# Kernel optimization log

Hardware: AMD Instinct MI355X
Metric: run time of the kernel (lower is better)

The kernel has to match this reference:

```python
import jax, jax.numpy as jnp
import numpy as np

B = 128          # graphs
N = 512          # nodes per graph
NT = B * N       # total nodes = 65536
E = NT * 16      # total edges = 1048576
IN = 64
H = 128
OUT = 2
L = 4            # num_layers
RATIO = 0.8


def setup_inputs() -> dict:
    key = jax.random.key(0)
    ks = jax.random.split(key, 20)

    def w(k, shape, fan_in):
        return jax.random.normal(k, shape, jnp.float32) / np.sqrt(fan_in)

    x = jax.random.normal(ks[0], (NT, IN), jnp.float32)
    edge_index = jax.random.randint(ks[1], (2, E), 0, NT, dtype=jnp.int32)
    batch = (jnp.arange(NT) // N).astype(jnp.int32)  # equal-size graphs

    return {
        "x": x,
        "edge_index": edge_index,
        "batch": batch,
        # conv1: GraphConv(IN, H, aggr='mean') -> lin_rel (w/ bias) + lin_root (no bias)
        "W1_rel": w(ks[2], (IN, H), IN),
        "W1_root": w(ks[3], (IN, H), IN),
        "b1": jnp.zeros((H,), jnp.float32),
        # convs[0..2]: GraphConv(H, H, aggr='mean'), stacked
        "Wc_rel": w(ks[4], (L - 1, H, H), H),
        "Wc_root": w(ks[5], (L - 1, H, H), H),
        "bc": jnp.zeros((L - 1, H), jnp.float32),
        # SAGPooling score GNN: GraphConv(H, 1) with default aggr='add'
        "pw_rel": w(ks[6], (H,), H),
        "pw_root": w(ks[7], (H,), H),
        "pb": jnp.zeros((1,), jnp.float32),
        # MLP head
        "lin1_W": w(ks[8], (L * H, H), L * H),
        "lin1_b": jnp.zeros((H,), jnp.float32),
        "lin2_W": w(ks[9], (H, OUT), H),
        "lin2_b": jnp.zeros((OUT,), jnp.float32),
    }


def _graph_conv_mean(x, src, dst, emask, W_rel, W_root, b, n):
    # PyG GraphConv: lin_rel(mean_{j->i} x_j) + lin_root(x_i); masked edges excluded.
    msg = x[src] * emask[:, None]                                  # [E, D] gather
    s = jax.ops.segment_sum(msg, dst, num_segments=n)              # [n, D] scatter-add
    cnt = jax.ops.segment_sum(emask, dst, num_segments=n)          # [n]
    agg = s / jnp.maximum(cnt, 1.0)[:, None]                       # zero for isolated nodes
    return agg @ W_rel + x @ W_root + b


def reference(x, edge_index, batch, W1_rel, W1_root, b1, Wc_rel, Wc_root, bc,
              pw_rel, pw_root, pb, lin1_W, lin1_b, lin2_W, lin2_b):
    src = edge_index[0]
    dst = edge_index[1]
    emask = jnp.ones((E,), jnp.float32)
    n = NT
    npg = N  # nodes per graph (all graphs equal size)

    h = jax.nn.relu(_graph_conv_mean(x, src, dst, emask, W1_rel, W1_root, b1, n))
    xs = [h.reshape(B, npg, H).mean(axis=1)]  # global_mean_pool

    for i in range(L - 1):
        h = jax.nn.relu(_graph_conv_mean(h, src, dst, emask, Wc_rel[i], Wc_root[i], bc[i], n))
        xs.append(h.reshape(B, npg, H).mean(axis=1))
        if i % 2 == 0 and i < L - 2:
            # ---- SAGPooling: score via GraphConv(H,1) with add aggregation ----
            smsg = jax.ops.segment_sum(h[src] * emask[:, None], dst, num_segments=n)
            score = smsg @ pw_rel + h @ pw_root + pb[0]            # [n]
            k = int(np.ceil(RATIO * npg))
            topv, topi = jax.lax.top_k(score.reshape(B, npg), k)   # per-graph top-k
            perm = (jnp.arange(B)[:, None] * npg + topi).reshape(-1)  # global kept ids
            h = h[perm] * jnp.tanh(topv.reshape(-1))[:, None]
            # remap edges; edges touching dropped nodes get masked out
            node_map = jnp.full((n,), -1, jnp.int32).at[perm].set(
                jnp.arange(B * k, dtype=jnp.int32))
            ns, nd = node_map[src], node_map[dst]
            keep = ((ns >= 0) & (nd >= 0)).astype(jnp.float32)
            emask = emask * keep
            src = jnp.where(ns >= 0, ns, 0)
            dst = jnp.where(nd >= 0, nd, 0)
            n = B * k
            npg = k

    xcat = jnp.concatenate(xs, axis=-1)                            # JumpingKnowledge 'cat'
    out = jax.nn.relu(xcat @ lin1_W + lin1_b)
    # dropout is identity in eval mode
    out = out @ lin2_W + lin2_b
    return jax.nn.log_softmax(out, axis=-1)
```

## Files before the change

kernel.cpp:

```cpp
#include <hip/hip_runtime.h>
#include <math.h>

#define NT 65536
#define EE 1048576
#define NB 128
#define KK 410
#define HH 128

typedef short bf16x8 __attribute__((ext_vector_type(8)));
typedef float f32x4 __attribute__((ext_vector_type(4)));

__device__ unsigned short g_xb[(size_t)NT * 64];
__device__ unsigned short g_hb1[(size_t)NT * HH];
__device__ unsigned short g_hb2[(size_t)NT * HH];
__device__ unsigned short g_aggb[(size_t)NT * HH];
__device__ unsigned short g_hpb[(size_t)NT * HH];
__device__ unsigned short g_aggb64[(size_t)NT * 64];
__device__ unsigned short g_wt1[128 * 128];
__device__ unsigned short g_wtc[3 * 128 * 256];
__device__ unsigned short g_csr1u[EE];
__device__ unsigned short g_keptu[NT];
__device__ unsigned int g_ebuck[EE];
__device__ int g_bcnt[128];
__device__ int g_bbase[129];
__device__ int g_bcur[128];
__device__ float g_trel[NT];
__device__ float g_troot[NT];
__device__ float g_score[NT];
__device__ float g_kinv[NT];
__device__ float g_xc4[4 * NB * 4 * 128];
__device__ int g_rows1[NT + 1];

__device__ __forceinline__ unsigned short* ubuf(int id) {
    switch (id) {
        case 0: return g_xb;
        case 1: return g_hb1;
        case 2: return g_hb2;
        case 3: return g_aggb;
        case 4: return g_hpb;
        case 5: return g_aggb64;
        case 6: return g_wt1;
        case 7: return g_wtc;
    }
    return g_xb;
}

__device__ __forceinline__ float b2f(unsigned short u) {
    union { unsigned int i; float f; } v;
    v.i = ((unsigned int)u) << 16;
    return v.f;
}
__device__ __forceinline__ unsigned short f2b(float f) {
    unsigned int x = __float_as_uint(f);
    unsigned int r = x + 0x7fffu + ((x >> 16) & 1u);
    return (unsigned short)(r >> 16);
}

__global__ void k_prep(const float* __restrict__ x,
                       const float* __restrict__ W1r, const float* __restrict__ W1o,
                       const float* __restrict__ Wcr, const float* __restrict__ Wco) {
    int tid = blockIdx.x * 256 + threadIdx.x;
    if (tid < 1048576) {
        float4 v = *(const float4*)&x[(size_t)tid * 4];
        unsigned int lo = (unsigned int)f2b(v.x) | ((unsigned int)f2b(v.y) << 16);
        unsigned int hi = (unsigned int)f2b(v.z) | ((unsigned int)f2b(v.w) << 16);
        *(uint2*)&g_xb[(size_t)tid * 4] = make_uint2(lo, hi);
    } else if (tid < 1048576 + 16384) {
        int r = tid - 1048576;
        int k = r & 127, n = r >> 7;
        float v = (k < 64) ? W1r[k * 128 + n] : W1o[(k - 64) * 128 + n];
        g_wt1[n * 128 + k] = f2b(v);
    } else if (tid < 1048576 + 16384 + 98304) {
        int r = tid - (1048576 + 16384);
        int l = r >> 15;
        int k = r & 255, n = (r >> 8) & 127;
        float v = (k < 128) ? Wcr[l * 16384 + k * 128 + n]
                            : Wco[l * 16384 + (k - 128) * 128 + n];
        g_wtc[l * 32768 + n * 256 + k] = f2b(v);
    } else if (tid < 1048576 + 16384 + 98304 + 128) {
        g_bcnt[tid - (1048576 + 16384 + 98304)] = 0;
    }
}

__global__ __launch_bounds__(256) void k_bhist(const int* __restrict__ dst) {
    __shared__ int h[128];
    if (threadIdx.x < 128) h[threadIdx.x] = 0;
    __syncthreads();
    int e0 = (blockIdx.x * 256 + threadIdx.x) * 4;
    int4 d = *(const int4*)&dst[e0];
    atomicAdd(&h[d.x >> 9], 1);
    atomicAdd(&h[d.y >> 9], 1);
    atomicAdd(&h[d.z >> 9], 1);
    atomicAdd(&h[d.w >> 9], 1);
    __syncthreads();
    if (threadIdx.x < 128 && h[threadIdx.x]) atomicAdd(&g_bcnt[threadIdx.x], h[threadIdx.x]);
}

__global__ __launch_bounds__(128) void k_bscan() {
    __shared__ int s[128];
    int t = threadIdx.x;
    int v = g_bcnt[t];
    s[t] = v;
    __syncthreads();
    for (int off = 1; off < 128; off <<= 1) {
        int u = (t >= off) ? s[t - off] : 0;
        __syncthreads();
        s[t] += u;
        __syncthreads();
    }
    g_bbase[t] = s[t] - v;
    g_bcur[t] = s[t] - v;
    if (t == 127) g_bbase[128] = s[127];
}

__global__ __launch_bounds__(256) void k_bscatter(const int* __restrict__ src,
                                                  const int* __restrict__ dst) {
    __shared__ int h[128];
    __shared__ int base[128];
    if (threadIdx.x < 128) h[threadIdx.x] = 0;
    __syncthreads();
    int e0 = (blockIdx.x * 256 + threadIdx.x) * 4;
    int4 s = *(const int4*)&src[e0];
    int4 d = *(const int4*)&dst[e0];
    int b0 = d.x >> 9, b1 = d.y >> 9, b2 = d.z >> 9, b3 = d.w >> 9;
    atomicAdd(&h[b0], 1);
    atomicAdd(&h[b1], 1);
    atomicAdd(&h[b2], 1);
    atomicAdd(&h[b3], 1);
    __syncthreads();
    if (threadIdx.x < 128) {
        int c = h[threadIdx.x];
        base[threadIdx.x] = c ? atomicAdd(&g_bcur[threadIdx.x], c) : 0;
        h[threadIdx.x] = 0;
    }
    __syncthreads();
    int r0 = atomicAdd(&h[b0], 1);
    g_ebuck[base[b0] + r0] = ((unsigned int)(d.x & 511) << 16) | (unsigned int)s.x;
    int r1 = atomicAdd(&h[b1], 1);
    g_ebuck[base[b1] + r1] = ((unsigned int)(d.y & 511) << 16) | (unsigned int)s.y;
    int r2 = atomicAdd(&h[b2], 1);
    g_ebuck[base[b2] + r2] = ((unsigned int)(d.z & 511) << 16) | (unsigned int)s.z;
    int r3 = atomicAdd(&h[b3], 1);
    g_ebuck[base[b3] + r3] = ((unsigned int)(d.w & 511) << 16) | (unsigned int)s.w;
}

__global__ __launch_bounds__(512) void k_bcsr() {
    __shared__ int hist[512];
    __shared__ int offs[512];
    __shared__ int cur[512];
    int g = blockIdx.x, t = threadIdx.x;
    hist[t] = 0;
    cur[t] = 0;
    __syncthreads();
    int b0 = g_bbase[g], b1 = g_bbase[g + 1];
    for (int e = b0 + t; e < b1; e += 512) {
        unsigned int p = g_ebuck[e];
        atomicAdd(&hist[p >> 16], 1);
    }
    __syncthreads();
    int v = hist[t];
    offs[t] = v;
    __syncthreads();
    for (int off = 1; off < 512; off <<= 1) {
        int u = (t >= off) ? offs[t - off] : 0;
        __syncthreads();
        offs[t] += u;
        __syncthreads();
    }
    int excl = offs[t] - v;
    g_rows1[g * 512 + t] = b0 + excl;
    if (t == 511) g_rows1[g * 512 + 512] = b0 + excl + v;
    __syncthreads();
    offs[t] = excl;
    __syncthreads();
    for (int e = b0 + t; e < b1; e += 512) {
        unsigned int p = g_ebuck[e];
        int dl = p >> 16;
        int r = atomicAdd(&cur[dl], 1);
        g_csr1u[b0 + offs[dl] + r] = (unsigned short)(p & 0xFFFFu);
    }
}

template <int D, int KC>
__global__ __launch_bounds__(256) void k_agg(int hId, int outId) {
    const unsigned short* h = ubuf(hId);
    unsigned short* out = ubuf(outId);
    const int TPN = D / 8;
    const int npb = 256 / TPN;
    int local = threadIdx.x / TPN;
    int t = threadIdx.x % TPN;
    int node = blockIdx.x * npb + local;
    int r0 = g_rows1[node], r1 = g_rows1[node + 1];
    float kinv_pre = (KC == 2) ? g_kinv[node] : 0.f;
    float acc[8];
#pragma unroll
    for (int i = 0; i < 8; i++) acc[i] = 0.f;
    int kc = 0;
    const unsigned short* ht = h + t * 8;
#define ACCV(v)                                                  \
    acc[0] += b2f((unsigned short)(v.x & 0xffff));               \
    acc[1] += b2f((unsigned short)(v.x >> 16));                  \
    acc[2] += b2f((unsigned short)(v.y & 0xffff));               \
    acc[3] += b2f((unsigned short)(v.y >> 16));                  \
    acc[4] += b2f((unsigned short)(v.z & 0xffff));               \
    acc[5] += b2f((unsigned short)(v.z >> 16));                  \
    acc[6] += b2f((unsigned short)(v.w & 0xffff));               \
    acc[7] += b2f((unsigned short)(v.w >> 16));
    int e = r0;
    for (; e + 8 <= r1; e += 8) {
        int i0 = g_csr1u[e], i1 = g_csr1u[e + 1], i2 = g_csr1u[e + 2], i3 = g_csr1u[e + 3];
        int i4 = g_csr1u[e + 4], i5 = g_csr1u[e + 5], i6 = g_csr1u[e + 6], i7 = g_csr1u[e + 7];
        uint4 v0 = *(const uint4*)&ht[(size_t)i0 * D];
        uint4 v1 = *(const uint4*)&ht[(size_t)i1 * D];
        uint4 v2 = *(const uint4*)&ht[(size_t)i2 * D];
        uint4 v3 = *(const uint4*)&ht[(size_t)i3 * D];
        uint4 v4 = *(const uint4*)&ht[(size_t)i4 * D];
        uint4 v5 = *(const uint4*)&ht[(size_t)i5 * D];
        uint4 v6 = *(const uint4*)&ht[(size_t)i6 * D];
        uint4 v7 = *(const uint4*)&ht[(size_t)i7 * D];
        if (KC == 1)
            kc += (int)g_keptu[i0] + (int)g_keptu[i1] + (int)g_keptu[i2] + (int)g_keptu[i3]
                + (int)g_keptu[i4] + (int)g_keptu[i5] + (int)g_keptu[i6] + (int)g_keptu[i7];
        ACCV(v0) ACCV(v1) ACCV(v2) ACCV(v3) ACCV(v4) ACCV(v5) ACCV(v6) ACCV(v7)
    }
    for (; e + 4 <= r1; e += 4) {
        int i0 = g_csr1u[e], i1 = g_csr1u[e + 1], i2 = g_csr1u[e + 2], i3 = g_csr1u[e + 3];
        uint4 v0 = *(const uint4*)&ht[(size_t)i0 * D];
        uint4 v1 = *(const uint4*)&ht[(size_t)i1 * D];
        uint4 v2 = *(const uint4*)&ht[(size_t)i2 * D];
        uint4 v3 = *(const uint4*)&ht[(size_t)i3 * D];
        if (KC == 1)
            kc += (int)g_keptu[i0] + (int)g_keptu[i1] + (int)g_keptu[i2] + (int)g_keptu[i3];
        ACCV(v0) ACCV(v1) ACCV(v2) ACCV(v3)
    }
    for (; e < r1; e++) {
        int i0 = g_csr1u[e];
        uint4 v0 = *(const uint4*)&ht[(size_t)i0 * D];
        if (KC == 1) kc += (int)g_keptu[i0];
        ACCV(v0)
    }
#undef ACCV
    float inv;
    if (KC == 0) {
        int c = r1 - r0;
        inv = 1.0f / (float)(c > 0 ? c : 1);
    } else if (KC == 1) {
        inv = 1.0f / (float)(kc > 0 ? kc : 1);
        if (t == 0) g_kinv[node] = inv;
    } else {
        inv = kinv_pre;
    }
    uint4 o;
    o.x = (unsigned int)f2b(acc[0] * inv) | ((unsigned int)f2b(acc[1] * inv) << 16);
    o.y = (unsigned int)f2b(acc[2] * inv) | ((unsigned int)f2b(acc[3] * inv) << 16);
    o.z = (unsigned int)f2b(acc[4] * inv) | ((unsigned int)f2b(acc[5] * inv) << 16);
    o.w = (unsigned int)f2b(acc[6] * inv) | ((unsigned int)f2b(acc[7] * inv) << 16);
    *(uint4*)&out[(size_t)node * D + t * 8] = o;
}

template <int KA, int KB, int MASKED, int DOTS>
__global__ __launch_bounds__(256) void k_mm(int aId, int bId, int wId, int wOfs,
                                            const float* __restrict__ bias, int outId,
                                            int sec,
                                            const float* __restrict__ pwr,
                                            const float* __restrict__ pwt) {
    const unsigned short* Ap = ubuf(aId);
    const unsigned short* Bp = ubuf(bId);
    const unsigned short* Wt = ubuf(wId) + wOfs;
    unsigned short* out = ubuf(outId);
    __shared__ float s[128];
    const int K = KA + KB;
    int lane = threadIdx.x & 63;
    int w = threadIdx.x >> 6;
    int n16 = lane & 15, quad = lane >> 4;
    int rowbase = blockIdx.x * 128 + w * 32;
    int g = blockIdx.x >> 2, qb = blockIdx.x & 3;
    f32x4 acc[2][8];
#pragma unroll
    for (int rt = 0; rt < 2; rt++)
#pragma unroll
        for (int ct = 0; ct < 8; ct++)
#pragma unroll
            for (int i = 0; i < 4; i++) acc[rt][ct][i] = 0.f;

#pragma unroll
    for (int ks = 0; ks < K / 32; ks++) {
        int k0 = ks * 32;
        const unsigned short* S;
        int kk, str;
        if (k0 < KA) { S = Ap; kk = k0; str = KA; }
        else         { S = Bp; kk = k0 - KA; str = KB; }
        bf16x8 a0 = *(const bf16x8*)&S[(size_t)(rowbase + n16) * str + kk + quad * 8];
        bf16x8 a1 = *(const bf16x8*)&S[(size_t)(rowbase + 16 + n16) * str + kk + quad * 8];
#pragma unroll
        for (int ct = 0; ct < 8; ct++) {
            bf16x8 b = *(const bf16x8*)&Wt[(size_t)(ct * 16 + n16) * K + k0 + quad * 8];
            acc[0][ct] = __builtin_amdgcn_mfma_f32_16x16x32_bf16(a0, b, acc[0][ct], 0, 0, 0);
            acc[1][ct] = __builtin_amdgcn_mfma_f32_16x16x32_bf16(a1, b, acc[1][ct], 0, 0, 0);
        }
    }

    if (threadIdx.x < 128) s[threadIdx.x] = 0.f;
#pragma unroll
    for (int rt = 0; rt < 2; rt++) {
        float m[4];
#pragma unroll
        for (int i = 0; i < 4; i++) {
            int r = rowbase + rt * 16 + quad * 4 + i;
            m[i] = (!MASKED || g_keptu[r]) ? 1.0f : 0.0f;
        }
#pragma unroll
        for (int ct = 0; ct < 8; ct++) {
            int c = ct * 16 + n16;
            float bv = bias[c];
#pragma unroll
            for (int i = 0; i < 4; i++) {
                int r = rowbase + rt * 16 + quad * 4 + i;
                float v = fmaxf(acc[rt][ct][i] + bv, 0.f) * m[i];
                acc[rt][ct][i] = v;
                out[(size_t)r * 128 + c] = f2b(v);
            }
        }
    }
    __syncthreads();

#pragma unroll
    for (int ct = 0; ct < 8; ct++) {
        float p = 0.f;
#pragma unroll
        for (int rt = 0; rt < 2; rt++)
#pragma unroll
            for (int i = 0; i < 4; i++) p += acc[rt][ct][i];
        p += __shfl_xor(p, 16);
        p += __shfl_xor(p, 32);
        if (quad == 0) atomicAdd(&s[ct * 16 + n16], p);
    }

    if (DOTS) {
        float pr[8], pt[8];
#pragma unroll
        for (int ct = 0; ct < 8; ct++) {
            pr[ct] = pwr[ct * 16 + n16];
            pt[ct] = pwt[ct * 16 + n16];
        }
#pragma unroll
        for (int rt = 0; rt < 2; rt++)
#pragma unroll
            for (int i = 0; i < 4; i++) {
                float dr = 0.f, dt = 0.f;
#pragma unroll
                for (int ct = 0; ct < 8; ct++) {
                    dr += acc[rt][ct][i] * pr[ct];
                    dt += acc[rt][ct][i] * pt[ct];
                }
                dr += __shfl_xor(dr, 1); dt += __shfl_xor(dt, 1);
                dr += __shfl_xor(dr, 2); dt += __shfl_xor(dt, 2);
                dr += __shfl_xor(dr, 4); dt += __shfl_xor(dt, 4);
                dr += __shfl_xor(dr, 8); dt += __shfl_xor(dt, 8);
                if (n16 == 0) {
                    int r = rowbase + rt * 16 + quad * 4 + i;
                    g_trel[r] = dr;
                    g_troot[r] = dt;
                }
            }
    }
    __syncthreads();
    if (threadIdx.x < 128)
        g_xc4[((sec * NB + g) * 4 + qb) * 128 + threadIdx.x] = s[threadIdx.x];
}

__global__ void k_score_agg(const float* __restrict__ pb) {
    int i = blockIdx.x * blockDim.x + threadIdx.x;
    if (i >= NT) return;
    int r0 = g_rows1[i], r1 = g_rows1[i + 1];
    float s = 0.f;
    int e = r0;
    for (; e + 4 <= r1; e += 4) {
        float s0 = g_trel[g_csr1u[e]];
        float s1 = g_trel[g_csr1u[e + 1]];
        float s2 = g_trel[g_csr1u[e + 2]];
        float s3 = g_trel[g_csr1u[e + 3]];
        s += (s0 + s1) + (s2 + s3);
    }
    for (; e < r1; e++) s += g_trel[g_csr1u[e]];
    g_score[i] = s + g_troot[i] + pb[0];
}

__global__ __launch_bounds__(256) void k_topk() {
    __shared__ float sv[512];
    __shared__ int si[512];
    __shared__ float gl[512];
    int g = blockIdx.x, t = threadIdx.x;
    for (int i = t; i < 512; i += 256) { sv[i] = g_score[g * 512 + i]; si[i] = i; }
    __syncthreads();
    for (int k = 2; k <= 512; k <<= 1) {
        for (int j = k >> 1; j > 0; j >>= 1) {
            for (int i = t; i < 512; i += 256) {
                int p = i ^ j;
                if (p > i) {
                    float va = sv[i], vb = sv[p];
                    int ia = si[i], ib = si[p];
                    bool aFirst = (va > vb) || (va == vb && ia < ib);
                    bool up = ((i & k) == 0);
                    if (up != aFirst) { sv[i] = vb; sv[p] = va; si[i] = ib; si[p] = ia; }
                }
            }
            __syncthreads();
        }
    }
    for (int r = t; r < 512; r += 256) {
        int lo = si[r];
        int old = g * 512 + lo;
        if (r < KK) {
            gl[lo] = tanhf(sv[r]);
            g_keptu[old] = 1;
        } else {
            gl[lo] = 0.f;
            g_keptu[old] = 0;
        }
    }
    __syncthreads();
    for (int idx = t; idx < 512 * 16; idx += 256) {
        int lr = idx >> 4, c = idx & 15;
        float gt = gl[lr];
        size_t off = (size_t)(g * 512 + lr) * 128 + c * 8;
        uint4 v = *(const uint4*)&g_hb2[off];
        uint4 o;
        o.x = (unsigned int)f2b(b2f((unsigned short)(v.x & 0xffff)) * gt) |
              ((unsigned int)f2b(b2f((unsigned short)(v.x >> 16)) * gt) << 16);
        o.y = (unsigned int)f2b(b2f((unsigned short)(v.y & 0xffff)) * gt) |
              ((unsigned int)f2b(b2f((unsigned short)(v.y >> 16)) * gt) << 16);
        o.z = (unsigned int)f2b(b2f((unsigned short)(v.z & 0xffff)) * gt) |
              ((unsigned int)f2b(b2f((unsigned short)(v.z >> 16)) * gt) << 16);
        o.w = (unsigned int)f2b(b2f((unsigned short)(v.w & 0xffff)) * gt) |
              ((unsigned int)f2b(b2f((unsigned short)(v.w >> 16)) * gt) << 16);
        *(uint4*)&g_hpb[off] = o;
    }
}

__global__ __launch_bounds__(128) void k_head(const float* __restrict__ W1, const float* __restrict__ b1,
                                              const float* __restrict__ W2, const float* __restrict__ b2,
                                              float* __restrict__ out) {
    __shared__ float xr[512];
    __shared__ float r0[128], r1[128];
    int g = blockIdx.x, t = threadIdx.x;
    for (int i = t; i < 512; i += 128) {
        int sec = i >> 7, c = i & 127;
        const float* p = &g_xc4[((sec * NB + g) * 4) * 128 + c];
        float v = p[0] + p[128] + p[256] + p[384];
        float inv = (sec < 2) ? (1.0f / 512.0f) : (1.0f / 410.0f);
        xr[i] = v * inv;
    }
    __syncthreads();
    float acc = b1[t];
    for (int k = 0; k < 512; k++) acc += xr[k] * W1[k * 128 + t];
    acc = fmaxf(acc, 0.f);
    r0[t] = acc * W2[t * 2 + 0];
    r1[t] = acc * W2[t * 2 + 1];
    __syncthreads();
    for (int off = 64; off > 0; off >>= 1) {
        if (t < off) { r0[t] += r0[t + off]; r1[t] += r1[t + off]; }
        __syncthreads();
    }
    if (t == 0) {
        float z0 = r0[0] + b2[0], z1 = r1[0] + b2[1];
        float m = fmaxf(z0, z1);
        float l = m + logf(expf(z0 - m) + expf(z1 - m));
        out[g * 2 + 0] = z0 - l;
        out[g * 2 + 1] = z1 - l;
    }
}

extern "C" void kernel_launch(void* const* d_in, const int* in_sizes, int n_in,
                              void* d_out, int out_size, void* d_ws, size_t ws_size,
                              hipStream_t stream) {
    const float* x = (const float*)d_in[0];
    const int* ei = (const int*)d_in[1];
    const int* src = ei;
    const int* dst = ei + EE;
    const float* W1r = (const float*)d_in[3];
    const float* W1o = (const float*)d_in[4];
    const float* b1 = (const float*)d_in[5];
    const float* Wcr = (const float*)d_in[6];
    const float* Wco = (const float*)d_in[7];
    const float* bc = (const float*)d_in[8];
    const float* pwr = (const float*)d_in[9];
    const float* pwt = (const float*)d_in[10];
    const float* pb = (const float*)d_in[11];
    const float* l1W = (const float*)d_in[12];
    const float* l1b = (const float*)d_in[13];
    const float* l2W = (const float*)d_in[14];
    const float* l2b = (const float*)d_in[15];
    float* out = (float*)d_out;

    k_prep<<<(1048576 + 16384 + 98304 + 128 + 255) / 256, 256, 0, stream>>>(x, W1r, W1o, Wcr, Wco);

    k_bhist<<<1024, 256, 0, stream>>>(dst);
    k_bscan<<<1, 128, 0, stream>>>();
    k_bscatter<<<1024, 256, 0, stream>>>(src, dst);
    k_bcsr<<<128, 512, 0, stream>>>();

    k_agg<64, 0><<<NT / 32, 256, 0, stream>>>(0, 5);
    k_mm<64, 64, 0, 0><<<NT / 128, 256, 0, stream>>>(5, 0, 6, 0, b1, 1, 0, pwr, pwt);

    k_agg<128, 0><<<NT / 16, 256, 0, stream>>>(1, 3);
    k_mm<128, 128, 0, 1><<<NT / 128, 256, 0, stream>>>(3, 1, 7, 0, bc, 2, 1, pwr, pwt);

    k_score_agg<<<NT / 256, 256, 0, stream>>>(pb);
    k_topk<<<NB, 256, 0, stream>>>();

    k_agg<128, 1><<<NT / 16, 256, 0, stream>>>(4, 3);
    k_mm<128, 128, 1, 0><<<NT / 128, 256, 0, stream>>>(3, 4, 7, 32768, bc + 128, 1, 2, pwr, pwt);

    k_agg<128, 2><<<NT / 16, 256, 0, stream>>>(1, 3);
    k_mm<128, 128, 1, 0><<<NT / 128, 256, 0, stream>>>(3, 1, 7, 65536, bc + 256, 2, 3, pwr, pwt);

    k_head<<<NB, 128, 0, stream>>>(l1W, l1b, l2W, l2b, out);
}
```

Before: 501.0 us.

## Fold SAGPool gate into aggregation and matmul, fuse score into topk, split agg by chunk

Removes the materialized gated feature buffer: top-k now writes a per-node gate factor, and the following aggregation and matmul apply the gate on the fly when reading neighbor and root features. The separate score-aggregation kernel is folded into the top-k kernel. The aggregation kernel is also restructured so that each block handles 64 nodes for a 32-column chunk, with 4 threads per node, and its 8-wide unroll is dropped. This saves a full write and read of the pooled features and one launch, at the cost of extra gate loads and multiplies in the gather loop, and a rounding order that differs slightly from before.

```diff
diff --git a/kernel.cpp b/kernel.cpp
--- a/kernel.cpp
+++ b/kernel.cpp
@@ -14,7 +14,6 @@
 __device__ unsigned short g_hb1[(size_t)NT * HH];
 __device__ unsigned short g_hb2[(size_t)NT * HH];
 __device__ unsigned short g_aggb[(size_t)NT * HH];
-__device__ unsigned short g_hpb[(size_t)NT * HH];
 __device__ unsigned short g_aggb64[(size_t)NT * 64];
 __device__ unsigned short g_wt1[128 * 128];
 __device__ unsigned short g_wtc[3 * 128 * 256];
@@ -26,7 +25,7 @@
 __device__ int g_bcur[128];
 __device__ float g_trel[NT];
 __device__ float g_troot[NT];
-__device__ float g_score[NT];
+__device__ float g_gatef[NT];
 __device__ float g_kinv[NT];
 __device__ float g_xc4[4 * NB * 4 * 128];
 __device__ int g_rows1[NT + 1];
@@ -37,10 +36,9 @@
         case 1: return g_hb1;
         case 2: return g_hb2;
         case 3: return g_aggb;
-        case 4: return g_hpb;
-        case 5: return g_aggb64;
-        case 6: return g_wt1;
-        case 7: return g_wtc;
+        case 4: return g_aggb64;
+        case 5: return g_wt1;
+        case 6: return g_wtc;
     }
     return g_xb;
 }
@@ -54,6 +52,15 @@
     unsigned int x = __float_as_uint(f);
     unsigned int r = x + 0x7fffu + ((x >> 16) & 1u);
     return (unsigned short)(r >> 16);
+}
+__device__ __forceinline__ bf16x8 scale8(bf16x8 a, float g) {
+    bf16x8 r;
+#pragma unroll
+    for (int i = 0; i < 8; i++) {
+        unsigned short u = (unsigned short)a[i];
+        r[i] = (short)f2b(b2f(u) * g);
+    }
+    return r;
 }
 
 __global__ void k_prep(const float* __restrict__ x,
@@ -181,63 +188,53 @@
     }
 }
 
-template <int D, int KC>
+template <int D, int KC, int GATED>
 __global__ __launch_bounds__(256) void k_agg(int hId, int outId) {
+    constexpr int NC = D / 32;
     const unsigned short* h = ubuf(hId);
     unsigned short* out = ubuf(outId);
-    const int TPN = D / 8;
-    const int npb = 256 / TPN;
-    int local = threadIdx.x / TPN;
-    int t = threadIdx.x % TPN;
-    int node = blockIdx.x * npb + local;
+    int chunk = blockIdx.x & (NC - 1);
+    int nodeg = blockIdx.x / NC;
+    int local = threadIdx.x >> 2;
+    int t = threadIdx.x & 3;
+    int node = nodeg * 64 + local;
     int r0 = g_rows1[node], r1 = g_rows1[node + 1];
     float kinv_pre = (KC == 2) ? g_kinv[node] : 0.f;
     float acc[8];
 #pragma unroll
     for (int i = 0; i < 8; i++) acc[i] = 0.f;
     int kc = 0;
-    const unsigned short* ht = h + t * 8;
-#define ACCV(v)                                                  \
-    acc[0] += b2f((unsigned short)(v.x & 0xffff));               \
-    acc[1] += b2f((unsigned short)(v.x >> 16));                  \
-    acc[2] += b2f((unsigned short)(v.y & 0xffff));               \
-    acc[3] += b2f((unsigned short)(v.y >> 16));                  \
-    acc[4] += b2f((unsigned short)(v.z & 0xffff));               \
-    acc[5] += b2f((unsigned short)(v.z >> 16));                  \
-    acc[6] += b2f((unsigned short)(v.w & 0xffff));               \
-    acc[7] += b2f((unsigned short)(v.w >> 16));
+    const unsigned short* ht = h + chunk * 32 + t * 8;
+#define ACCV(v, gf)                                              \
+    acc[0] += gf * b2f((unsigned short)(v.x & 0xffff));          \
+    acc[1] += gf * b2f((unsigned short)(v.x >> 16));             \
+    acc[2] += gf * b2f((unsigned short)(v.y & 0xffff));          \
+    acc[3] += gf * b2f((unsigned short)(v.y >> 16));             \
+    acc[4] += gf * b2f((unsigned short)(v.z & 0xffff));          \
+    acc[5] += gf * b2f((unsigned short)(v.z >> 16));             \
+    acc[6] += gf * b2f((unsigned short)(v.w & 0xffff));          \
+    acc[7] += gf * b2f((unsigned short)(v.w >> 16));
     int e = r0;
-    for (; e + 8 <= r1; e += 8) {
-        int i0 = g_csr1u[e], i1 = g_csr1u[e + 1], i2 = g_csr1u[e + 2], i3 = g_csr1u[e + 3];
-        int i4 = g_csr1u[e + 4], i5 = g_csr1u[e + 5], i6 = g_csr1u[e + 6], i7 = g_csr1u[e + 7];
-        uint4 v0 = *(const uint4*)&ht[(size_t)i0 * D];
-        uint4 v1 = *(const uint4*)&ht[(size_t)i1 * D];
-        uint4 v2 = *(const uint4*)&ht[(size_t)i2 * D];
-        uint4 v3 = *(const uint4*)&ht[(size_t)i3 * D];
-        uint4 v4 = *(const uint4*)&ht[(size_t)i4 * D];
-        uint4 v5 = *(const uint4*)&ht[(size_t)i5 * D];
-        uint4 v6 = *(const uint4*)&ht[(size_t)i6 * D];
-        uint4 v7 = *(const uint4*)&ht[(size_t)i7 * D];
-        if (KC == 1)
-            kc += (int)g_keptu[i0] + (int)g_keptu[i1] + (int)g_keptu[i2] + (int)g_keptu[i3]
-                + (int)g_keptu[i4] + (int)g_keptu[i5] + (int)g_keptu[i6] + (int)g_keptu[i7];
-        ACCV(v0) ACCV(v1) ACCV(v2) ACCV(v3) ACCV(v4) ACCV(v5) ACCV(v6) ACCV(v7)
-    }
     for (; e + 4 <= r1; e += 4) {
         int i0 = g_csr1u[e], i1 = g_csr1u[e + 1], i2 = g_csr1u[e + 2], i3 = g_csr1u[e + 3];
         uint4 v0 = *(const uint4*)&ht[(size_t)i0 * D];
         uint4 v1 = *(const uint4*)&ht[(size_t)i1 * D];
         uint4 v2 = *(const uint4*)&ht[(size_t)i2 * D];
         uint4 v3 = *(const uint4*)&ht[(size_t)i3 * D];
+        float g0 = GATED ? g_gatef[i0] : 1.0f;
+        float g1 = GATED ? g_gatef[i1] : 1.0f;
+        float g2 = GATED ? g_gatef[i2] : 1.0f;
+        float g3 = GATED ? g_gatef[i3] : 1.0f;
         if (KC == 1)
             kc += (int)g_keptu[i0] + (int)g_keptu[i1] + (int)g_keptu[i2] + (int)g_keptu[i3];
-        ACCV(v0) ACCV(v1) ACCV(v2) ACCV(v3)
+        ACCV(v0, g0) ACCV(v1, g1) ACCV(v2, g2) ACCV(v3, g3)
     }
     for (; e < r1; e++) {
         int i0 = g_csr1u[e];
         uint4 v0 = *(const uint4*)&ht[(size_t)i0 * D];
+        float g0 = GATED ? g_gatef[i0] : 1.0f;
         if (KC == 1) kc += (int)g_keptu[i0];
-        ACCV(v0)
+        ACCV(v0, g0)
     }
 #undef ACCV
     float inv;
@@ -255,10 +252,10 @@
     o.y = (unsigned int)f2b(acc[2] * inv) | ((unsigned int)f2b(acc[3] * inv) << 16);
     o.z = (unsigned int)f2b(acc[4] * inv) | ((unsigned int)f2b(acc[5] * inv) << 16);
     o.w = (unsigned int)f2b(acc[6] * inv) | ((unsigned int)f2b(acc[7] * inv) << 16);
-    *(uint4*)&out[(size_t)node * D + t * 8] = o;
-}
-
-template <int KA, int KB, int MASKED, int DOTS>
+    *(uint4*)&out[(size_t)node * D + chunk * 32 + t * 8] = o;
+}
+
+template <int KA, int KB, int MASKED, int DOTS, int BGATE>
 __global__ __launch_bounds__(256) void k_mm(int aId, int bId, int wId, int wOfs,
                                             const float* __restrict__ bias, int outId,
                                             int sec,
@@ -275,6 +272,8 @@
     int n16 = lane & 15, quad = lane >> 4;
     int rowbase = blockIdx.x * 128 + w * 32;
     int g = blockIdx.x >> 2, qb = blockIdx.x & 3;
+    float ga0 = BGATE ? g_gatef[rowbase + n16] : 1.0f;
+    float ga1 = BGATE ? g_gatef[rowbase + 16 + n16] : 1.0f;
     f32x4 acc[2][8];
 #pragma unroll
     for (int rt = 0; rt < 2; rt++)
@@ -292,6 +291,10 @@
         else         { S = Bp; kk = k0 - KA; str = KB; }
         bf16x8 a0 = *(const bf16x8*)&S[(size_t)(rowbase + n16) * str + kk + quad * 8];
         bf16x8 a1 = *(const bf16x8*)&S[(size_t)(rowbase + 16 + n16) * str + kk + quad * 8];
+        if (BGATE && k0 >= KA) {
+            a0 = scale8(a0, ga0);
+            a1 = scale8(a1, ga1);
+        }
 #pragma unroll
         for (int ct = 0; ct < 8; ct++) {
             bf16x8 b = *(const bf16x8*)&Wt[(size_t)(ct * 16 + n16) * K + k0 + quad * 8];
@@ -369,29 +372,27 @@
         g_xc4[((sec * NB + g) * 4 + qb) * 128 + threadIdx.x] = s[threadIdx.x];
 }
 
-__global__ void k_score_agg(const float* __restrict__ pb) {
-    int i = blockIdx.x * blockDim.x + threadIdx.x;
-    if (i >= NT) return;
-    int r0 = g_rows1[i], r1 = g_rows1[i + 1];
-    float s = 0.f;
-    int e = r0;
-    for (; e + 4 <= r1; e += 4) {
-        float s0 = g_trel[g_csr1u[e]];
-        float s1 = g_trel[g_csr1u[e + 1]];
-        float s2 = g_trel[g_csr1u[e + 2]];
-        float s3 = g_trel[g_csr1u[e + 3]];
-        s += (s0 + s1) + (s2 + s3);
-    }
-    for (; e < r1; e++) s += g_trel[g_csr1u[e]];
-    g_score[i] = s + g_troot[i] + pb[0];
-}
-
-__global__ __launch_bounds__(256) void k_topk() {
+__global__ __launch_bounds__(256) void k_topk(const float* __restrict__ pb) {
     __shared__ float sv[512];
     __shared__ int si[512];
-    __shared__ float gl[512];
     int g = blockIdx.x, t = threadIdx.x;
-    for (int i = t; i < 512; i += 256) { sv[i] = g_score[g * 512 + i]; si[i] = i; }
+    float pbv = pb[0];
+    for (int l = t; l < 512; l += 256) {
+        int node = g * 512 + l;
+        int r0 = g_rows1[node], r1 = g_rows1[node + 1];
+        float s = 0.f;
+        int e = r0;
+        for (; e + 4 <= r1; e += 4) {
+            float s0 = g_trel[g_csr1u[e]];
+            float s1 = g_trel[g_csr1u[e + 1]];
+            float s2 = g_trel[g_csr1u[e + 2]];
+            float s3 = g_trel[g_csr1u[e + 3]];
+            s += (s0 + s1) + (s2 + s3);
+        }
+        for (; e < r1; e++) s += g_trel[g_csr1u[e]];
+        sv[l] = s + g_troot[node] + pbv;
+        si[l] = l;
+    }
     __syncthreads();
     for (int k = 2; k <= 512; k <<= 1) {
         for (int j = k >> 1; j > 0; j >>= 1) {
@@ -409,32 +410,14 @@
         }
     }
     for (int r = t; r < 512; r += 256) {
-        int lo = si[r];
-        int old = g * 512 + lo;
+        int old = g * 512 + si[r];
         if (r < KK) {
-            gl[lo] = tanhf(sv[r]);
+            g_gatef[old] = tanhf(sv[r]);
             g_keptu[old] = 1;
         } else {
-            gl[lo] = 0.f;
+            g_gatef[old] = 0.f;
             g_keptu[old] = 0;
         }
-    }
-    __syncthreads();
-    for (int idx = t; idx < 512 * 16; idx += 256) {
-        int lr = idx >> 4, c = idx & 15;
-        float gt = gl[lr];
-        size_t off = (size_t)(g * 512 + lr) * 128 + c * 8;
-        uint4 v = *(const uint4*)&g_hb2[off];
-        uint4 o;
-        o.x = (unsigned int)f2b(b2f((unsigned short)(v.x & 0xffff)) * gt) |
-              ((unsigned int)f2b(b2f((unsigned short)(v.x >> 16)) * gt) << 16);
-        o.y = (unsigned int)f2b(b2f((unsigned short)(v.y & 0xffff)) * gt) |
-              ((unsigned int)f2b(b2f((unsigned short)(v.y >> 16)) * gt) << 16);
-        o.z = (unsigned int)f2b(b2f((unsigned short)(v.z & 0xffff)) * gt) |
-              ((unsigned int)f2b(b2f((unsigned short)(v.z >> 16)) * gt) << 16);
-        o.w = (unsigned int)f2b(b2f((unsigned short)(v.w & 0xffff)) * gt) |
-              ((unsigned int)f2b(b2f((unsigned short)(v.w >> 16)) * gt) << 16);
-        *(uint4*)&g_hpb[off] = o;
     }
 }
 
@@ -500,20 +483,19 @@
     k_bscatter<<<1024, 256, 0, stream>>>(src, dst);
     k_bcsr<<<128, 512, 0, stream>>>();
 
-    k_agg<64, 0><<<NT / 32, 256, 0, stream>>>(0, 5);
-    k_mm<64, 64, 0, 0><<<NT / 128, 256, 0, stream>>>(5, 0, 6, 0, b1, 1, 0, pwr, pwt);
-
-    k_agg<128, 0><<<NT / 16, 256, 0, stream>>>(1, 3);
-    k_mm<128, 128, 0, 1><<<NT / 128, 256, 0, stream>>>(3, 1, 7, 0, bc, 2, 1, pwr, pwt);
-
-    k_score_agg<<<NT / 256, 256, 0, stream>>>(pb);
-    k_topk<<<NB, 256, 0, stream>>>();
-
-    k_agg<128, 1><<<NT / 16, 256, 0, stream>>>(4, 3);
-    k_mm<128, 128, 1, 0><<<NT / 128, 256, 0, stream>>>(3, 4, 7, 32768, bc + 128, 1, 2, pwr, pwt);
-
-    k_agg<128, 2><<<NT / 16, 256, 0, stream>>>(1, 3);
-    k_mm<128, 128, 1, 0><<<NT / 128, 256, 0, stream>>>(3, 1, 7, 65536, bc + 256, 2, 3, pwr, pwt);
+    k_agg<64, 0, 0><<<2048, 256, 0, stream>>>(0, 4);
+    k_mm<64, 64, 0, 0, 0><<<512, 256, 0, stream>>>(4, 0, 5, 0, b1, 1, 0, pwr, pwt);
+
+    k_agg<128, 0, 0><<<4096, 256, 0, stream>>>(1, 3);
+    k_mm<128, 128, 0, 1, 0><<<512, 256, 0, stream>>>(3, 1, 6, 0, bc, 2, 1, pwr, pwt);
+
+    k_topk<<<NB, 256, 0, stream>>>(pb);
+
+    k_agg<128, 1, 1><<<4096, 256, 0, stream>>>(2, 3);
+    k_mm<128, 128, 1, 0, 1><<<512, 256, 0, stream>>>(3, 2, 6, 32768, bc + 128, 1, 2, pwr, pwt);
+
+    k_agg<128, 2, 0><<<4096, 256, 0, stream>>>(1, 3);
+    k_mm<128, 128, 1, 0, 0><<<512, 256, 0, stream>>>(3, 1, 6, 65536, bc + 256, 2, 3, pwr, pwt);
 
     k_head<<<NB, 128, 0, stream>>>(l1W, l1b, l2W, l2b, out);
 }
```

Measured after the change: 680.8 us. 1.36x slower.
